# Kernel optimization log

Hardware: AMD Instinct MI355X
Metric: run time of the kernel (lower is better)

## Reference

```python
import jax, jax.numpy as jnp
import numpy as np

N = 100000      # nodes
E = 1600000     # directed edges (avg degree 16)
D_IN, D_H, D_OUT = 128, 128, 1


def gcn_conv(x, src, dst, W, b, n):
    """PyG GCNConv: out = D^{-1/2} (A+I) D^{-1/2} X W + b.
    src/dst already include self-loops. deg counted on dst (in-degree)."""
    h = x @ W                                            # [n, d_out]
    deg = jax.ops.segment_sum(jnp.ones(src.shape[0], h.dtype), dst, num_segments=n)
    dinv = jax.lax.rsqrt(jnp.maximum(deg, 1.0))          # deg >= 1 (self loops)
    norm = dinv[src] * dinv[dst]                         # [e]
    msg = h[src] * norm[:, None]                         # gather + scale, [e, d_out]
    out = jax.ops.segment_sum(msg, dst, num_segments=n)  # scatter-add, [n, d_out]
    return out + b


def setup_inputs() -> dict:
    key = jax.random.key(0)
    ks = jax.random.split(key, 8)
    x = jax.random.normal(ks[0], (N, D_IN), dtype=jnp.float32)
    edge_index = jax.random.randint(ks[1], (2, E), 0, N, dtype=jnp.int64)

    def glorot(k, fan_in, fan_out):
        s = jnp.sqrt(6.0 / (fan_in + fan_out)).astype(jnp.float32)
        return jax.random.uniform(k, (fan_in, fan_out), jnp.float32, -s, s)

    W0 = glorot(ks[2], D_IN, D_H)
    b0 = jnp.zeros((D_H,), jnp.float32)
    W1 = glorot(ks[3], D_H, D_H)
    b1 = jnp.zeros((D_H,), jnp.float32)
    W2 = glorot(ks[4], D_H, D_OUT)
    b2 = jnp.zeros((D_OUT,), jnp.float32)
    return {"x": x, "edge_index": edge_index,
            "W0": W0, "b0": b0, "W1": W1, "b1": b1, "W2": W2, "b2": b2}


def reference(x, edge_index, W0, b0, W1, b1, W2, b2):
    n = x.shape[0]
    loops = jnp.arange(n, dtype=edge_index.dtype)
    src = jnp.concatenate([edge_index[0], loops])
    dst = jnp.concatenate([edge_index[1], loops])
    # dropout is identity in eval mode
    h = jax.nn.relu(gcn_conv(x, src, dst, W0, b0, n))
    h = jax.nn.relu(gcn_conv(h, src, dst, W1, b1, n))
    out = gcn_conv(h, src, dst, W2, b2, n)
    return jax.nn.sigmoid(out)
```

## Files before the change

kernel.cpp:

```cpp
#include <hip/hip_runtime.h>
#include <cstddef>

#define D 128
#define BW_LOG 9
#define BW 512
#define CHUNK 8192
#define GP 136
typedef unsigned int uint;
typedef unsigned short ushort;

typedef __attribute__((ext_vector_type(8))) short bf16x8;
typedef __attribute__((ext_vector_type(4))) float f32x4;
typedef __attribute__((ext_vector_type(2))) float f32x2;

static __device__ __forceinline__ uint bf16r(float x) {
  uint u = __float_as_uint(x);
  return (u + 0x7fffu + ((u >> 16) & 1u)) >> 16;
}
static __device__ __forceinline__ uint pack2(float a, float b) {
  return bf16r(a) | (bf16r(b) << 16);
}
static __device__ __forceinline__ void accp(uint w, f32x2* a) {
  f32x2 t;
  t.x = __uint_as_float(w << 16);
  t.y = __uint_as_float(w & 0xffff0000u);
  *a += t;
}
static __device__ __forceinline__ void acc_bf16x8p(const uint4 v, f32x2* a) {
  accp(v.x, a + 0);
  accp(v.y, a + 1);
  accp(v.z, a + 2);
  accp(v.w, a + 3);
}

__global__ void k_wsplit(const float* __restrict__ W0, const float* __restrict__ W1,
                         ushort* __restrict__ out, int* __restrict__ bcnt) {
  int idx = blockIdx.x * 256 + threadIdx.x;
  if (idx < 256) bcnt[idx] = 0;
  if (idx >= 32768) return;
  int lay = idx >> 14;
  int rem = idx & 16383;
  int col = rem >> 7, k = rem & 127;
  const float* W = lay ? W1 : W0;
  float w = W[k * D + col];
  uint hb = bf16r(w);
  float hf = __uint_as_float(hb << 16);
  out[lay * 32768 + rem] = (ushort)hb;
  out[lay * 32768 + 16384 + rem] = (ushort)bf16r(w - hf);
}

__global__ __launch_bounds__(512)
void k_bhist(const int* __restrict__ dstA, int* __restrict__ bcnt, int e, int nb) {
  __shared__ int h[256];
  int t = threadIdx.x;
  if (t < 256) h[t] = 0;
  __syncthreads();
  int base = blockIdx.x * CHUNK;
  int m = min(CHUNK, e - base);
  for (int i = t; i < m; i += 512) atomicAdd(&h[dstA[base + i] >> BW_LOG], 1);
  __syncthreads();
  if (t < nb && h[t]) atomicAdd(&bcnt[t], h[t]);
}

__global__ void k_bscan(const int* __restrict__ bcnt, int* __restrict__ bbase,
                        int* __restrict__ cursor, int* __restrict__ off,
                        int nb, int n, int e) {
  __shared__ int s[256];
  int t = threadIdx.x;
  int v = (t < nb) ? bcnt[t] : 0;
  s[t] = v;
  __syncthreads();
  for (int d = 1; d < 256; d <<= 1) {
    int x = (t >= d) ? s[t - d] : 0;
    __syncthreads();
    s[t] += x;
    __syncthreads();
  }
  if (t < nb) {
    int b = s[t] - v;
    bbase[t] = b;
    cursor[t] = b;
  }
  if (t == 0) {
    bbase[nb] = e;
    off[n] = e;
  }
}

__global__ __launch_bounds__(512)
void k_bscatter(const int* __restrict__ ei, int* __restrict__ cursor,
                int* __restrict__ pk, int e, int nb) {
  __shared__ int h[256], s2[256], gpos[256], lcur[256];
  __shared__ int staged[CHUNK];
  int t = threadIdx.x;
  if (t < 256) h[t] = 0;
  __syncthreads();
  int base = blockIdx.x * CHUNK;
  int m = min(CHUNK, e - base);
  int sv[16], dv[16];
#pragma unroll
  for (int k = 0; k < 16; ++k) {
    int i = t + k * 512;
    sv[k] = 0; dv[k] = 0;
    if (i < m) {
      sv[k] = ei[base + i];
      dv[k] = ei[e + base + i];
      atomicAdd(&h[dv[k] >> BW_LOG], 1);
    }
  }
  __syncthreads();
  if (t < 256) s2[t] = h[t];
  __syncthreads();
  for (int d = 1; d < 256; d <<= 1) {
    int x = 0;
    if (t < 256 && t >= d) x = s2[t - d];
    __syncthreads();
    if (t < 256) s2[t] += x;
    __syncthreads();
  }
  if (t < 256) {
    lcur[t] = s2[t] - h[t];
    gpos[t] = (t < nb && h[t]) ? atomicAdd(&cursor[t], h[t]) : 0;
  }
  __syncthreads();
#pragma unroll
  for (int k = 0; k < 16; ++k) {
    int i = t + k * 512;
    if (i < m) {
      int b = dv[k] >> BW_LOG;
      int p = atomicAdd(&lcur[b], 1);
      staged[p] = sv[k] | ((dv[k] & (BW - 1)) << 17);
    }
  }
  __syncthreads();
  for (int i = t; i < m; i += 512) {
    int lo = 0, hi = nb;
    while (lo < hi) {
      int mid = (lo + hi) >> 1;
      if (s2[mid] <= i) lo = mid + 1; else hi = mid;
    }
    int lb = s2[lo] - h[lo];
    pk[gpos[lo] + (i - lb)] = staged[i];
  }
}

__global__ __launch_bounds__(1024)
void k_bfinal(const int* __restrict__ bbase, const int* __restrict__ pk,
              int* __restrict__ off, float* __restrict__ dinv,
              int* __restrict__ csr, int n, int nb) {
  __shared__ int sc[BW];
  __shared__ int lcur[BW];
  const int b = blockIdx.x;
  const int t = threadIdx.x;
  const int e0 = bbase[b], e1 = bbase[b + 1];
  const int node0 = b << BW_LOG;
  if (t < BW) { sc[t] = 0; lcur[t] = 0; }
  __syncthreads();
  for (int i = e0 + t; i < e1; i += 1024) atomicAdd(&sc[(pk[i] >> 17) & (BW - 1)], 1);
  __syncthreads();
  int c0 = (t < BW) ? sc[t] : 0;
  for (int d = 1; d < BW; d <<= 1) {
    int v0 = (t < BW && t >= d) ? sc[t - d] : 0;
    __syncthreads();
    if (t < BW) sc[t] += v0;
    __syncthreads();
  }
  if (t < BW) {
    int na = node0 + t;
    if (na < n) {
      off[na] = e0 + sc[t] - c0;
      dinv[na] = rsqrtf((float)c0 + 1.0f);
    }
    sc[t] -= c0;
  }
  __syncthreads();
  for (int i = e0 + t; i < e1; i += 1024) {
    int v = pk[i];
    int dl = (v >> 17) & (BW - 1);
    int p = atomicAdd(&lcur[dl], 1);
    csr[e0 + sc[dl] + p] = v & 0x1FFFF;
  }
}

template <bool BF16A>
__global__ __launch_bounds__(256)
void k_mgemm(const void* __restrict__ Xv, const ushort* __restrict__ Wht,
             const ushort* __restrict__ Wlt, const float* __restrict__ dinv,
             ushort* __restrict__ Asb, int n, int nstrips) {
  __shared__ __align__(16) ushort Wh[128 * GP];
  const int tid = threadIdx.x;

  for (int c = tid; c < 2048; c += 256)
    *(uint4*)(&Wh[(c >> 4) * GP + (c & 15) * 8]) = *(const uint4*)(Wht + c * 8);
  __syncthreads();

  const int wv = tid >> 6;
  const int l = tid & 63;
  const int lr = l & 15;
  const int lk = (l >> 4) * 8;

  const float* Xf = (const float*)Xv;
  const ushort* Xb = (const ushort*)Xv;

  for (int strip = blockIdx.x * 4 + wv; strip < nstrips; strip += gridDim.x * 4) {
    const int row0 = strip * 16;
    f32x4 acc[8];
#pragma unroll
    for (int t = 0; t < 8; ++t) acc[t] = (f32x4){0.f, 0.f, 0.f, 0.f};

    const int arow = row0 + lr;
    const bool av = (arow < n);

#pragma unroll
    for (int ks = 0; ks < 4; ++ks) {
      const int k0 = ks * 32 + lk;
      bf16x8 ahv;
      if (BF16A) {
        if (av) {
          ahv = *(const bf16x8*)(Xb + (size_t)arow * D + k0);
        } else {
          union { bf16x8 v; ushort a[8]; } z;
#pragma unroll
          for (int j = 0; j < 8; ++j) z.a[j] = 0;
          ahv = z.v;
        }
      } else {
        union { bf16x8 v; ushort a[8]; } ah;
        if (av) {
          const f32x4* ap = (const f32x4*)(Xf + (size_t)arow * D + k0);
          f32x4 u0 = __builtin_nontemporal_load(ap);
          f32x4 u1 = __builtin_nontemporal_load(ap + 1);
          ah.a[0] = (ushort)bf16r(u0.x);
          ah.a[1] = (ushort)bf16r(u0.y);
          ah.a[2] = (ushort)bf16r(u0.z);
          ah.a[3] = (ushort)bf16r(u0.w);
          ah.a[4] = (ushort)bf16r(u1.x);
          ah.a[5] = (ushort)bf16r(u1.y);
          ah.a[6] = (ushort)bf16r(u1.z);
          ah.a[7] = (ushort)bf16r(u1.w);
        } else {
#pragma unroll
          for (int j = 0; j < 8; ++j) ah.a[j] = 0;
        }
        ahv = ah.v;
      }
#pragma unroll
      for (int nt = 0; nt < 8; ++nt) {
        bf16x8 bh = *(const bf16x8*)(&Wh[(nt * 16 + lr) * GP + k0]);
        bf16x8 bl = *(const bf16x8*)(Wlt + (size_t)(nt * 16 + lr) * D + k0);
        acc[nt] = __builtin_amdgcn_mfma_f32_16x16x32_bf16(ahv, bh, acc[nt], 0, 0, 0);
        acc[nt] = __builtin_amdgcn_mfma_f32_16x16x32_bf16(ahv, bl, acc[nt], 0, 0, 0);
      }
    }

#pragma unroll
    for (int r = 0; r < 4; ++r) {
      int row = row0 + (l >> 4) * 4 + r;
      if (row < n) {
        float di = dinv[row];
#pragma unroll
        for (int nt = 0; nt < 8; ++nt) {
          Asb[(size_t)row * D + nt * 16 + lr] = (ushort)bf16r(acc[nt][r] * di);
        }
      }
    }
  }
}

template <bool FUSE_DOT>
__global__ __launch_bounds__(256)
void k_gather(const int* __restrict__ off, const int* __restrict__ csr,
              const float* __restrict__ dinv, const ushort* __restrict__ Asb,
              ushort* __restrict__ Bb, const float* __restrict__ bias,
              const float* __restrict__ W2, float* __restrict__ ss, int n) {
  const int wid = blockIdx.x * 4 + (threadIdx.x >> 6);
  if (wid >= n) return;
  const int lane = threadIdx.x & 63;
  const int q = lane >> 4;
  const int li = lane & 15;
  const int c = li << 3;

  f32x2 a2[4];
#pragma unroll
  for (int k = 0; k < 4; ++k) a2[k] = (f32x2){0.f, 0.f};
  if (q == 0) {
    uint4 sv = *(const uint4*)(Asb + (size_t)wid * D + c);
    acc_bf16x8p(sv, a2);
  }

  const int o0 = off[wid], o1 = off[wid + 1];
  for (int j0 = o0; j0 < o1; j0 += 64) {
    int sj = 0;
    if (j0 + lane < o1) sj = csr[j0 + lane];
    const int m = min(64, o1 - j0);
    const int nst = (m + 3) >> 2;
#pragma unroll 4
    for (int t = 0; t < nst; ++t) {
      int idx = (t << 2) + q;
      int s = __shfl(sj, idx);
      if (idx < m) {
        uint4 v = *(const uint4*)(Asb + (size_t)s * D + c);
        acc_bf16x8p(v, a2);
      }
    }
  }

  float a[8];
#pragma unroll
  for (int k = 0; k < 4; ++k) { a[2 * k] = a2[k].x; a[2 * k + 1] = a2[k].y; }
#pragma unroll
  for (int k = 0; k < 8; ++k) {
    a[k] += __shfl_xor(a[k], 16);
    a[k] += __shfl_xor(a[k], 32);
  }

  const float di = dinv[wid];
  float4 bb0 = *(const float4*)(bias + c);
  float4 bb1 = *(const float4*)(bias + c + 4);
  float v0 = fmaxf(a[0] * di + bb0.x, 0.f);
  float v1 = fmaxf(a[1] * di + bb0.y, 0.f);
  float v2 = fmaxf(a[2] * di + bb0.z, 0.f);
  float v3 = fmaxf(a[3] * di + bb0.w, 0.f);
  float v4 = fmaxf(a[4] * di + bb1.x, 0.f);
  float v5 = fmaxf(a[5] * di + bb1.y, 0.f);
  float v6 = fmaxf(a[6] * di + bb1.z, 0.f);
  float v7 = fmaxf(a[7] * di + bb1.w, 0.f);

  if (FUSE_DOT) {
    float4 w0 = *(const float4*)(W2 + c);
    float4 w1 = *(const float4*)(W2 + c + 4);
    float p = v0 * w0.x + v1 * w0.y + v2 * w0.z + v3 * w0.w +
              v4 * w1.x + v5 * w1.y + v6 * w1.z + v7 * w1.w;
    p += __shfl_xor(p, 1);
    p += __shfl_xor(p, 2);
    p += __shfl_xor(p, 4);
    p += __shfl_xor(p, 8);
    if (lane == 0) ss[wid] = p * di;
  } else {
    if (lane < 16) {
      uint4 w;
      w.x = pack2(v0, v1);
      w.y = pack2(v2, v3);
      w.z = pack2(v4, v5);
      w.w = pack2(v6, v7);
      *(uint4*)(Bb + (size_t)wid * D + c) = w;
    }
  }
}

__global__ void k_gather_scalar(const int* __restrict__ off, const int* __restrict__ csr,
                                const float* __restrict__ dinv, const float* __restrict__ ss,
                                const float* __restrict__ b2, float* __restrict__ out, int n) {
  int i = blockIdx.x * 256 + threadIdx.x;
  if (i >= n) return;
  float acc = ss[i];
  int j = off[i], o1 = off[i + 1];
  float a0 = 0.f, a1 = 0.f, a2 = 0.f, a3 = 0.f;
  for (; j + 4 <= o1; j += 4) {
    int s0 = csr[j], s1 = csr[j + 1], s2 = csr[j + 2], s3 = csr[j + 3];
    a0 += ss[s0];
    a1 += ss[s1];
    a2 += ss[s2];
    a3 += ss[s3];
  }
  for (; j < o1; ++j) a0 += ss[csr[j]];
  acc += (a0 + a1) + (a2 + a3);
  float v = acc * dinv[i] + b2[0];
  out[i] = 1.f / (1.f + expf(-v));
}

extern "C" void kernel_launch(void* const* d_in, const int* in_sizes, int n_in,
                              void* d_out, int out_size, void* d_ws, size_t ws_size,
                              hipStream_t stream) {
  const float* x  = (const float*)d_in[0];
  const int*   ei = (const int*)d_in[1];
  const float* W0 = (const float*)d_in[2];
  const float* b0 = (const float*)d_in[3];
  const float* W1 = (const float*)d_in[4];
  const float* b1 = (const float*)d_in[5];
  const float* W2 = (const float*)d_in[6];
  const float* b2 = (const float*)d_in[7];
  float* out = (float*)d_out;

  const int n = in_sizes[0] / D;
  const int e = in_sizes[1] / 2;
  const int nb = (n + BW - 1) / BW;
  const int nstrips = (n + 15) / 16;
  const size_t np = ((size_t)n + 256) / 256 * 256;

  float* ws = (float*)d_ws;
  int*    off    = (int*)ws;
  float*  dinv   = ws + np;
  float*  ss     = ws + 2 * np;
  int*    bmeta  = (int*)(ws + 3 * np);
  int*    bcnt   = bmeta;
  int*    bbase  = bmeta + 260;
  int*    cursor = bmeta + 600;
  ushort* wsp    = (ushort*)(ws + 3 * np + 1024);
  int*    csr    = (int*)(ws + 3 * np + 1024 + 32768);
  int*    pk     = csr + e;
  ushort* Asb    = (ushort*)(pk + e);
  ushort* Bb     = Asb + (size_t)n * D;

  const ushort* W0h = wsp;
  const ushort* W0l = wsp + 16384;
  const ushort* W1h = wsp + 32768;
  const ushort* W1l = wsp + 49152;

  const int g256n = (n + 255) / 256;
  const int ggath = (n + 3) / 4;
  const int gchnk = (e + CHUNK - 1) / CHUNK;
  const int ggemm = (nstrips + 3) / 4 < 1024 ? (nstrips + 3) / 4 : 1024;

  k_wsplit<<<128, 256, 0, stream>>>(W0, W1, (ushort*)wsp, bcnt);
  k_bhist<<<gchnk, 512, 0, stream>>>(ei + e, bcnt, e, nb);
  k_bscan<<<1, 256, 0, stream>>>(bcnt, bbase, cursor, off, nb, n, e);
  k_bscatter<<<gchnk, 512, 0, stream>>>(ei, cursor, pk, e, nb);
  k_bfinal<<<nb, 1024, 0, stream>>>(bbase, pk, off, dinv, csr, n, nb);

  k_mgemm<false><<<ggemm, 256, 0, stream>>>(x, W0h, W0l, dinv, Asb, n, nstrips);
  k_gather<false><<<ggath, 256, 0, stream>>>(off, csr, dinv, Asb, Bb, b0, nullptr, nullptr, n);

  k_mgemm<true><<<ggemm, 256, 0, stream>>>(Bb, W1h, W1l, dinv, Asb, n, nstrips);
  k_gather<true><<<ggath, 256, 0, stream>>>(off, csr, dinv, Asb, nullptr, b1, W2, ss, n);

  k_gather_scalar<<<g256n, 256, 0, stream>>>(off, csr, dinv, ss, b2, out, n);
}
```

Measured before the change: 283.4 us.

## Quantize gathered node features to per-row int8 with scale and permuted columns

The GEMM epilogue now writes each transformed row as 8-bit unsigned codes with a per-row absmax scale instead of bf16. The edge gather then reads 8 bytes per lane instead of 16 and dequantizes with an FMA plus a summed-scale correction. The column order changes to a lane-contiguous permutation, so biases, W2 and the W1 k-index are permuted to match. This roughly halves the bytes moved by the bandwidth-bound random gathers, at the cost of int8 quantization error and an extra scale load per edge.

```diff
diff --git a/kernel.cpp b/kernel.cpp
--- a/kernel.cpp
+++ b/kernel.cpp
@@ -8,10 +8,10 @@
 #define GP 136
 typedef unsigned int uint;
 typedef unsigned short ushort;
+typedef unsigned char uchar;
 
 typedef __attribute__((ext_vector_type(8))) short bf16x8;
 typedef __attribute__((ext_vector_type(4))) float f32x4;
-typedef __attribute__((ext_vector_type(2))) float f32x2;
 
 static __device__ __forceinline__ uint bf16r(float x) {
   uint u = __float_as_uint(x);
@@ -20,23 +20,29 @@
 static __device__ __forceinline__ uint pack2(float a, float b) {
   return bf16r(a) | (bf16r(b) << 16);
 }
-static __device__ __forceinline__ void accp(uint w, f32x2* a) {
-  f32x2 t;
-  t.x = __uint_as_float(w << 16);
-  t.y = __uint_as_float(w & 0xffff0000u);
-  *a += t;
-}
-static __device__ __forceinline__ void acc_bf16x8p(const uint4 v, f32x2* a) {
-  accp(v.x, a + 0);
-  accp(v.y, a + 1);
-  accp(v.z, a + 2);
-  accp(v.w, a + 3);
+static __device__ __forceinline__ void acc_u8x8(const uint2 v, float rs, float* a) {
+  a[0] = fmaf((float)(v.x & 0xffu), rs, a[0]);
+  a[1] = fmaf((float)((v.x >> 8) & 0xffu), rs, a[1]);
+  a[2] = fmaf((float)((v.x >> 16) & 0xffu), rs, a[2]);
+  a[3] = fmaf((float)(v.x >> 24), rs, a[3]);
+  a[4] = fmaf((float)(v.y & 0xffu), rs, a[4]);
+  a[5] = fmaf((float)((v.y >> 8) & 0xffu), rs, a[5]);
+  a[6] = fmaf((float)((v.y >> 16) & 0xffu), rs, a[6]);
+  a[7] = fmaf((float)(v.y >> 24), rs, a[7]);
 }
 
 __global__ void k_wsplit(const float* __restrict__ W0, const float* __restrict__ W1,
-                         ushort* __restrict__ out, int* __restrict__ bcnt) {
+                         const float* __restrict__ b0, const float* __restrict__ b1,
+                         const float* __restrict__ W2, ushort* __restrict__ out,
+                         float* __restrict__ bp, int* __restrict__ bcnt) {
   int idx = blockIdx.x * 256 + threadIdx.x;
   if (idx < 256) bcnt[idx] = 0;
+  if (idx < 128) {
+    int p = (idx & 15) * 8 + (idx >> 4);
+    bp[p] = b0[idx];
+    bp[128 + p] = b1[idx];
+    bp[256 + p] = W2[idx];
+  }
   if (idx >= 32768) return;
   int lay = idx >> 14;
   int rem = idx & 16383;
@@ -45,8 +51,9 @@
   float w = W[k * D + col];
   uint hb = bf16r(w);
   float hf = __uint_as_float(hb << 16);
-  out[lay * 32768 + rem] = (ushort)hb;
-  out[lay * 32768 + 16384 + rem] = (ushort)bf16r(w - hf);
+  int ks = lay ? ((k & 15) * 8 + (k >> 4)) : k;
+  out[lay * 32768 + col * 128 + ks] = (ushort)hb;
+  out[lay * 32768 + 16384 + col * 128 + ks] = (ushort)bf16r(w - hf);
 }
 
 __global__ __launch_bounds__(512)
@@ -186,7 +193,7 @@
 __global__ __launch_bounds__(256)
 void k_mgemm(const void* __restrict__ Xv, const ushort* __restrict__ Wht,
              const ushort* __restrict__ Wlt, const float* __restrict__ dinv,
-             ushort* __restrict__ Asb, int n, int nstrips) {
+             uchar* __restrict__ Aq, float* __restrict__ rs, int n, int nstrips) {
   __shared__ __align__(16) ushort Wh[128 * GP];
   const int tid = threadIdx.x;
 
@@ -256,12 +263,27 @@
 #pragma unroll
     for (int r = 0; r < 4; ++r) {
       int row = row0 + (l >> 4) * 4 + r;
+      float di = (row < n) ? dinv[row] : 0.f;
+      float v[8];
+      float am = 0.f;
+#pragma unroll
+      for (int nt = 0; nt < 8; ++nt) {
+        v[nt] = acc[nt][r] * di;
+        am = fmaxf(am, fabsf(v[nt]));
+      }
+      am = fmaxf(am, __shfl_xor(am, 1));
+      am = fmaxf(am, __shfl_xor(am, 2));
+      am = fmaxf(am, __shfl_xor(am, 4));
+      am = fmaxf(am, __shfl_xor(am, 8));
+      float inv = (am > 0.f) ? 127.f / am : 0.f;
+      uint q[8];
+#pragma unroll
+      for (int nt = 0; nt < 8; ++nt) q[nt] = (uint)(int)rintf(fmaf(v[nt], inv, 128.f));
+      uint w0 = q[0] | (q[1] << 8) | (q[2] << 16) | (q[3] << 24);
+      uint w1 = q[4] | (q[5] << 8) | (q[6] << 16) | (q[7] << 24);
       if (row < n) {
-        float di = dinv[row];
-#pragma unroll
-        for (int nt = 0; nt < 8; ++nt) {
-          Asb[(size_t)row * D + nt * 16 + lr] = (ushort)bf16r(acc[nt][r] * di);
-        }
+        *(uint2*)(Aq + (size_t)row * D + lr * 8) = make_uint2(w0, w1);
+        if (lr == 0) rs[row] = am * (1.f / 127.f);
       }
     }
   }
@@ -270,9 +292,10 @@
 template <bool FUSE_DOT>
 __global__ __launch_bounds__(256)
 void k_gather(const int* __restrict__ off, const int* __restrict__ csr,
-              const float* __restrict__ dinv, const ushort* __restrict__ Asb,
-              ushort* __restrict__ Bb, const float* __restrict__ bias,
-              const float* __restrict__ W2, float* __restrict__ ss, int n) {
+              const float* __restrict__ dinv, const uchar* __restrict__ Aq,
+              const float* __restrict__ rsc, ushort* __restrict__ Bb,
+              const float* __restrict__ bias, const float* __restrict__ W2,
+              float* __restrict__ ss, int n) {
   const int wid = blockIdx.x * 4 + (threadIdx.x >> 6);
   if (wid >= n) return;
   const int lane = threadIdx.x & 63;
@@ -280,12 +303,16 @@
   const int li = lane & 15;
   const int c = li << 3;
 
-  f32x2 a2[4];
-#pragma unroll
-  for (int k = 0; k < 4; ++k) a2[k] = (f32x2){0.f, 0.f};
+  float a[8];
+#pragma unroll
+  for (int k = 0; k < 8; ++k) a[k] = 0.f;
+  float ssc = 0.f;
+
   if (q == 0) {
-    uint4 sv = *(const uint4*)(Asb + (size_t)wid * D + c);
-    acc_bf16x8p(sv, a2);
+    uint2 sv = *(const uint2*)(Aq + (size_t)wid * D + c);
+    float rs = rsc[wid];
+    acc_u8x8(sv, rs, a);
+    ssc += rs;
   }
 
   const int o0 = off[wid], o1 = off[wid + 1];
@@ -299,15 +326,16 @@
       int idx = (t << 2) + q;
       int s = __shfl(sj, idx);
       if (idx < m) {
-        uint4 v = *(const uint4*)(Asb + (size_t)s * D + c);
-        acc_bf16x8p(v, a2);
+        uint2 v = *(const uint2*)(Aq + (size_t)s * D + c);
+        float rs = rsc[s];
+        acc_u8x8(v, rs, a);
+        ssc += rs;
       }
     }
   }
 
-  float a[8];
-#pragma unroll
-  for (int k = 0; k < 4; ++k) { a[2 * k] = a2[k].x; a[2 * k + 1] = a2[k].y; }
+#pragma unroll
+  for (int k = 0; k < 8; ++k) a[k] = fmaf(-128.f, ssc, a[k]);
 #pragma unroll
   for (int k = 0; k < 8; ++k) {
     a[k] += __shfl_xor(a[k], 16);
@@ -384,6 +412,7 @@
 
   const int n = in_sizes[0] / D;
   const int e = in_sizes[1] / 2;
+  const int ep = (e + 3) & ~3;
   const int nb = (n + BW - 1) / BW;
   const int nstrips = (n + 15) / 16;
   const size_t np = ((size_t)n + 256) / 256 * 256;
@@ -397,32 +426,39 @@
   int*    bbase  = bmeta + 260;
   int*    cursor = bmeta + 600;
   ushort* wsp    = (ushort*)(ws + 3 * np + 1024);
-  int*    csr    = (int*)(ws + 3 * np + 1024 + 32768);
-  int*    pk     = csr + e;
-  ushort* Asb    = (ushort*)(pk + e);
-  ushort* Bb     = Asb + (size_t)n * D;
+  float*  bp     = ws + 3 * np + 1024 + 32768;
+  int*    csr    = (int*)(bp + 512);
+  int*    pk     = csr + ep;
+  uchar*  Aq0    = (uchar*)(pk + ep);
+  float*  rs0    = (float*)(Aq0 + (size_t)n * D);
+  ushort* Bb     = (ushort*)(rs0 + np);
+  uchar*  Aq1    = (uchar*)(Bb + (size_t)n * D);
+  float*  rs1    = (float*)(Aq1 + (size_t)n * D);
 
   const ushort* W0h = wsp;
   const ushort* W0l = wsp + 16384;
   const ushort* W1h = wsp + 32768;
   const ushort* W1l = wsp + 49152;
+  const float*  b0p = bp;
+  const float*  b1p = bp + 128;
+  const float*  W2p = bp + 256;
 
   const int g256n = (n + 255) / 256;
   const int ggath = (n + 3) / 4;
   const int gchnk = (e + CHUNK - 1) / CHUNK;
   const int ggemm = (nstrips + 3) / 4 < 1024 ? (nstrips + 3) / 4 : 1024;
 
-  k_wsplit<<<128, 256, 0, stream>>>(W0, W1, (ushort*)wsp, bcnt);
+  k_wsplit<<<128, 256, 0, stream>>>(W0, W1, b0, b1, W2, (ushort*)wsp, bp, bcnt);
   k_bhist<<<gchnk, 512, 0, stream>>>(ei + e, bcnt, e, nb);
   k_bscan<<<1, 256, 0, stream>>>(bcnt, bbase, cursor, off, nb, n, e);
   k_bscatter<<<gchnk, 512, 0, stream>>>(ei, cursor, pk, e, nb);
   k_bfinal<<<nb, 1024, 0, stream>>>(bbase, pk, off, dinv, csr, n, nb);
 
-  k_mgemm<false><<<ggemm, 256, 0, stream>>>(x, W0h, W0l, dinv, Asb, n, nstrips);
-  k_gather<false><<<ggath, 256, 0, stream>>>(off, csr, dinv, Asb, Bb, b0, nullptr, nullptr, n);
-
-  k_mgemm<true><<<ggemm, 256, 0, stream>>>(Bb, W1h, W1l, dinv, Asb, n, nstrips);
-  k_gather<true><<<ggath, 256, 0, stream>>>(off, csr, dinv, Asb, nullptr, b1, W2, ss, n);
+  k_mgemm<false><<<ggemm, 256, 0, stream>>>(x, W0h, W0l, dinv, Aq0, rs0, n, nstrips);
+  k_gather<false><<<ggath, 256, 0, stream>>>(off, csr, dinv, Aq0, rs0, Bb, b0p, nullptr, nullptr, n);
+
+  k_mgemm<true><<<ggemm, 256, 0, stream>>>(Bb, W1h, W1l, dinv, Aq1, rs1, n, nstrips);
+  k_gather<true><<<ggath, 256, 0, stream>>>(off, csr, dinv, Aq1, rs1, nullptr, b1p, W2p, ss, n);
 
   k_gather_scalar<<<g256n, 256, 0, stream>>>(off, csr, dinv, ss, b2, out, n);
 }
```

Measured after the change: 279.7 us. No clear change (-1.3%).
